# Kernel tuning notes

Hardware: AMD Instinct MI355X
Metric: run time of the kernel (lower is better)

## Reference

```python
import jax, jax.numpy as jnp
import numpy as np


def setup_inputs() -> dict:
    key = jax.random.key(0)
    k1, k2 = jax.random.split(key)
    B, T, D = 16, 4096, 512
    x = jax.random.normal(k1, (B, T, D), dtype=jnp.float32)
    alpha = jax.random.normal(k2, (1, 1, D), dtype=jnp.float32)  # raw param, pre-sigmoid
    return {"x": x, "alpha": alpha}


def reference(x, alpha):
    # s_0 = x_0 ; s_t = a * x_t + (1 - a) * s_{t-1}, a = sigmoid(alpha)
    a = jax.nn.sigmoid(alpha[0, 0, :])  # (D,)
    one_minus_a = 1.0 - a

    def step(prev, xt):  # prev, xt: (B, D)
        cur = a * xt + one_minus_a * prev
        return cur, cur

    x_t = jnp.swapaxes(x, 0, 1)  # (T, B, D)
    init = x_t[0]
    _, rest = jax.lax.scan(step, init, x_t[1:])  # (T-1, B, D)
    states = jnp.concatenate([x_t[:1], rest], axis=0)  # (T, B, D)
    return jnp.swapaxes(states, 0, 1)  # (B, T, D)
```

## Files before the change

kernel.cpp:

```cpp
#include <hip/hip_runtime.h>
#include <math.h>

#define BB 16
#define TT 4096
#define DD 512
#define D4 128

__device__ __forceinline__ float sigmf(float v) {
    return 1.0f / (1.0f + expf(-v));
}

__global__ __launch_bounds__(256) void es_chunk_ends(
    const float* __restrict__ x, const float* __restrict__ alpha,
    float* __restrict__ ends, int C, int L)
{
    const int c   = blockIdx.x;
    const int tid = threadIdx.x;
    const int b   = (blockIdx.y << 1) + (tid >> 7);
    const int d4  = tid & 127;

    const float4 al = reinterpret_cast<const float4*>(alpha)[d4];
    const float ax = sigmf(al.x), ay = sigmf(al.y), az = sigmf(al.z), aw = sigmf(al.w);
    const float fx = 1.0f - ax, fy = 1.0f - ay, fz = 1.0f - az, fw = 1.0f - aw;

    const float4* xp = reinterpret_cast<const float4*>(x)
                     + ((size_t)b * TT + (size_t)c * L) * D4 + d4;

    float4 s;
    if (c == 0) {
        s = xp[0];
    } else {
        s.x = s.y = s.z = s.w = 0.0f;
    }

    #pragma unroll 8
    for (int i = 0; i < L; ++i) {
        const float4 v = xp[(size_t)i * D4];
        s.x = fmaf(ax, v.x, fx * s.x);
        s.y = fmaf(ay, v.y, fy * s.y);
        s.z = fmaf(az, v.z, fz * s.z);
        s.w = fmaf(aw, v.w, fw * s.w);
    }

    reinterpret_cast<float4*>(ends)[((size_t)b * C + c) * D4 + d4] = s;
}

__global__ __launch_bounds__(256) void es_carry_scan(
    float* __restrict__ ends, const float* __restrict__ alpha, int C, int L)
{
    const int g  = blockIdx.x * 256 + threadIdx.x;
    const int b  = g >> 7;
    const int d4 = g & 127;

    const float4 al = reinterpret_cast<const float4*>(alpha)[d4];
    const float ax = sigmf(al.x), ay = sigmf(al.y), az = sigmf(al.z), aw = sigmf(al.w);
    float4 fL;
    fL.x = powf(1.0f - ax, (float)L);
    fL.y = powf(1.0f - ay, (float)L);
    fL.z = powf(1.0f - az, (float)L);
    fL.w = powf(1.0f - aw, (float)L);

    float4* e = reinterpret_cast<float4*>(ends) + (size_t)b * C * D4 + d4;

    float4 S = e[0];
    int c = 1;
    for (; c + 8 <= C; c += 8) {
        float4 v[8];
        #pragma unroll
        for (int j = 0; j < 8; ++j) v[j] = e[(size_t)(c + j) * D4];
        #pragma unroll
        for (int j = 0; j < 8; ++j) {
            S.x = fmaf(fL.x, S.x, v[j].x);
            S.y = fmaf(fL.y, S.y, v[j].y);
            S.z = fmaf(fL.z, S.z, v[j].z);
            S.w = fmaf(fL.w, S.w, v[j].w);
            e[(size_t)(c + j) * D4] = S;
        }
    }
    for (; c < C; ++c) {
        const float4 v = e[(size_t)c * D4];
        S.x = fmaf(fL.x, S.x, v.x);
        S.y = fmaf(fL.y, S.y, v.y);
        S.z = fmaf(fL.z, S.z, v.z);
        S.w = fmaf(fL.w, S.w, v.w);
        e[(size_t)c * D4] = S;
    }
}

__global__ __launch_bounds__(256) void es_final(
    const float* __restrict__ x, const float* __restrict__ alpha,
    const float* __restrict__ finals, float* __restrict__ out, int C, int L)
{
    const int c   = blockIdx.x;
    const int tid = threadIdx.x;
    const int b   = (blockIdx.y << 1) + (tid >> 7);
    const int d4  = tid & 127;

    const float4 al = reinterpret_cast<const float4*>(alpha)[d4];
    const float ax = sigmf(al.x), ay = sigmf(al.y), az = sigmf(al.z), aw = sigmf(al.w);
    const float fx = 1.0f - ax, fy = 1.0f - ay, fz = 1.0f - az, fw = 1.0f - aw;

    const size_t base = ((size_t)b * TT + (size_t)c * L) * D4 + d4;
    const float4* xp = reinterpret_cast<const float4*>(x) + base;
    float4*       op = reinterpret_cast<float4*>(out) + base;

    float4 s;
    if (c == 0) {
        s = xp[0];
    } else {
        s = reinterpret_cast<const float4*>(finals)[((size_t)b * C + (c - 1)) * D4 + d4];
    }

    #pragma unroll 8
    for (int i = 0; i < L; ++i) {
        const float4 v = xp[(size_t)i * D4];
        s.x = fmaf(ax, v.x, fx * s.x);
        s.y = fmaf(ay, v.y, fy * s.y);
        s.z = fmaf(az, v.z, fz * s.z);
        s.w = fmaf(aw, v.w, fw * s.w);
        op[(size_t)i * D4] = s;
    }
}

__global__ __launch_bounds__(256) void es_serial(
    const float* __restrict__ x, const float* __restrict__ alpha,
    float* __restrict__ out)
{
    const int g  = blockIdx.x * 256 + threadIdx.x;
    const int b  = g >> 7;
    const int d4 = g & 127;

    const float4 al = reinterpret_cast<const float4*>(alpha)[d4];
    const float ax = sigmf(al.x), ay = sigmf(al.y), az = sigmf(al.z), aw = sigmf(al.w);
    const float fx = 1.0f - ax, fy = 1.0f - ay, fz = 1.0f - az, fw = 1.0f - aw;

    const float4* xp = reinterpret_cast<const float4*>(x) + (size_t)b * TT * D4 + d4;
    float4*       op = reinterpret_cast<float4*>(out) + (size_t)b * TT * D4 + d4;

    float4 s = xp[0];
    #pragma unroll 4
    for (int t = 0; t < TT; ++t) {
        const float4 v = xp[(size_t)t * D4];
        s.x = fmaf(ax, v.x, fx * s.x);
        s.y = fmaf(ay, v.y, fy * s.y);
        s.z = fmaf(az, v.z, fz * s.z);
        s.w = fmaf(aw, v.w, fw * s.w);
        op[(size_t)t * D4] = s;
    }
}

extern "C" void kernel_launch(void* const* d_in, const int* in_sizes, int n_in,
                              void* d_out, int out_size, void* d_ws, size_t ws_size,
                              hipStream_t stream)
{
    const float* x     = (const float*)d_in[0];
    const float* alpha = (const float*)d_in[1];
    float*       out   = (float*)d_out;

    int C = 128;
    while (C > 8 && (size_t)BB * C * DD * sizeof(float) > ws_size) C >>= 1;

    if ((size_t)BB * C * DD * sizeof(float) > ws_size) {
        es_serial<<<dim3(8), 256, 0, stream>>>(x, alpha, out);
        return;
    }

    const int L = TT / C;
    float* ends = (float*)d_ws;

    es_chunk_ends<<<dim3(C, BB / 2), 256, 0, stream>>>(x, alpha, ends, C, L);
    es_carry_scan<<<dim3(8), 256, 0, stream>>>(ends, alpha, C, L);
    es_final<<<dim3(C, BB / 2), 256, 0, stream>>>(x, alpha, ends, out, C, L);
}
```

Baseline: 269.0 us.

## Fuse carry scan into final pass and use nontemporal output stores

Removes the separate serial carry-scan kernel (8 blocks) by having each chunk block in the final pass recompute its own incoming carry, scanning the preceding chunk ends. This eliminates one launch and a poorly parallel serial stage, but adds redundant work that grows with chunk index (up to C-1 reads of ends per thread). Output stores are also switched to nontemporal stores to reduce cache pollution on the streaming write.

```diff
diff --git a/kernel.cpp b/kernel.cpp
--- a/kernel.cpp
+++ b/kernel.cpp
@@ -6,8 +6,15 @@
 #define DD 512
 #define D4 128
 
+typedef float v4f __attribute__((ext_vector_type(4)));
+
 __device__ __forceinline__ float sigmf(float v) {
     return 1.0f / (1.0f + expf(-v));
+}
+
+__device__ __forceinline__ void nt_store4(float4* p, const float4& s) {
+    __builtin_nontemporal_store(*reinterpret_cast<const v4f*>(&s),
+                                reinterpret_cast<v4f*>(p));
 }
 
 __global__ __launch_bounds__(256) void es_chunk_ends(
@@ -45,51 +52,9 @@
     reinterpret_cast<float4*>(ends)[((size_t)b * C + c) * D4 + d4] = s;
 }
 
-__global__ __launch_bounds__(256) void es_carry_scan(
-    float* __restrict__ ends, const float* __restrict__ alpha, int C, int L)
-{
-    const int g  = blockIdx.x * 256 + threadIdx.x;
-    const int b  = g >> 7;
-    const int d4 = g & 127;
-
-    const float4 al = reinterpret_cast<const float4*>(alpha)[d4];
-    const float ax = sigmf(al.x), ay = sigmf(al.y), az = sigmf(al.z), aw = sigmf(al.w);
-    float4 fL;
-    fL.x = powf(1.0f - ax, (float)L);
-    fL.y = powf(1.0f - ay, (float)L);
-    fL.z = powf(1.0f - az, (float)L);
-    fL.w = powf(1.0f - aw, (float)L);
-
-    float4* e = reinterpret_cast<float4*>(ends) + (size_t)b * C * D4 + d4;
-
-    float4 S = e[0];
-    int c = 1;
-    for (; c + 8 <= C; c += 8) {
-        float4 v[8];
-        #pragma unroll
-        for (int j = 0; j < 8; ++j) v[j] = e[(size_t)(c + j) * D4];
-        #pragma unroll
-        for (int j = 0; j < 8; ++j) {
-            S.x = fmaf(fL.x, S.x, v[j].x);
-            S.y = fmaf(fL.y, S.y, v[j].y);
-            S.z = fmaf(fL.z, S.z, v[j].z);
-            S.w = fmaf(fL.w, S.w, v[j].w);
-            e[(size_t)(c + j) * D4] = S;
-        }
-    }
-    for (; c < C; ++c) {
-        const float4 v = e[(size_t)c * D4];
-        S.x = fmaf(fL.x, S.x, v.x);
-        S.y = fmaf(fL.y, S.y, v.y);
-        S.z = fmaf(fL.z, S.z, v.z);
-        S.w = fmaf(fL.w, S.w, v.w);
-        e[(size_t)c * D4] = S;
-    }
-}
-
-__global__ __launch_bounds__(256) void es_final(
+__global__ __launch_bounds__(256) void es_final_fused(
     const float* __restrict__ x, const float* __restrict__ alpha,
-    const float* __restrict__ finals, float* __restrict__ out, int C, int L)
+    const float* __restrict__ ends, float* __restrict__ out, int C, int L)
 {
     const int c   = blockIdx.x;
     const int tid = threadIdx.x;
@@ -108,7 +73,37 @@
     if (c == 0) {
         s = xp[0];
     } else {
-        s = reinterpret_cast<const float4*>(finals)[((size_t)b * C + (c - 1)) * D4 + d4];
+        float4 fL;
+        fL.x = powf(fx, (float)L);
+        fL.y = powf(fy, (float)L);
+        fL.z = powf(fz, (float)L);
+        fL.w = powf(fw, (float)L);
+
+        const float4* e = reinterpret_cast<const float4*>(ends)
+                        + (size_t)b * C * D4 + d4;
+
+        float4 S = e[0];
+        int j = 1;
+        for (; j + 8 <= c; j += 8) {
+            float4 v[8];
+            #pragma unroll
+            for (int k = 0; k < 8; ++k) v[k] = e[(size_t)(j + k) * D4];
+            #pragma unroll
+            for (int k = 0; k < 8; ++k) {
+                S.x = fmaf(fL.x, S.x, v[k].x);
+                S.y = fmaf(fL.y, S.y, v[k].y);
+                S.z = fmaf(fL.z, S.z, v[k].z);
+                S.w = fmaf(fL.w, S.w, v[k].w);
+            }
+        }
+        for (; j < c; ++j) {
+            const float4 v = e[(size_t)j * D4];
+            S.x = fmaf(fL.x, S.x, v.x);
+            S.y = fmaf(fL.y, S.y, v.y);
+            S.z = fmaf(fL.z, S.z, v.z);
+            S.w = fmaf(fL.w, S.w, v.w);
+        }
+        s = S;
     }
 
     #pragma unroll 8
@@ -118,7 +113,7 @@
         s.y = fmaf(ay, v.y, fy * s.y);
         s.z = fmaf(az, v.z, fz * s.z);
         s.w = fmaf(aw, v.w, fw * s.w);
-        op[(size_t)i * D4] = s;
+        nt_store4(op + (size_t)i * D4, s);
     }
 }
 
@@ -169,6 +164,5 @@
     float* ends = (float*)d_ws;
 
     es_chunk_ends<<<dim3(C, BB / 2), 256, 0, stream>>>(x, alpha, ends, C, L);
-    es_carry_scan<<<dim3(8), 256, 0, stream>>>(ends, alpha, C, L);
-    es_final<<<dim3(C, BB / 2), 256, 0, stream>>>(x, alpha, ends, out, C, L);
+    es_final_fused<<<dim3(C, BB / 2), 256, 0, stream>>>(x, alpha, ends, out, C, L);
 }
```

Result: faster. 261.5 us (-2.8%).
